# Kernel tuning notes

Measured on AMD Instinct MI355X. Metric: run time of the kernel, lower is better.

The kernel has to match this reference:

```python
import jax, jax.numpy as jnp
import numpy as np

B, S, N, H, E = 512, 96, 64, 512, 512  # batch, seq_len, nodes(c_in), hidden, edges/graph


def setup_inputs() -> dict:
    key = jax.random.key(0)
    ks = jax.random.split(key, 6)
    x = jax.random.normal(ks[0], (B, S, N), jnp.float32)
    edge_index = jax.random.randint(ks[1], (B, 2, E), 0, N, dtype=jnp.int32)
    W1 = jax.random.normal(ks[2], (H, S), jnp.float32) * 0.05   # gcn1 lin weight [out,in]
    b1 = jnp.zeros((H,), jnp.float32)
    W2 = jax.random.normal(ks[3], (S, H), jnp.float32) * 0.05   # gcn2 lin weight
    b2 = jnp.zeros((S,), jnp.float32)
    conv_w = jax.random.normal(ks[4], (H, N, 3), jnp.float32) * 0.05  # Conv1d [out,in,k]
    return {"x": x, "edge_index": edge_index, "W1": W1, "b1": b1,
            "W2": W2, "b2": b2, "conv_w": conv_w}


def _gcn(h, src, dst, W, b, n):
    # PyG GCNConv: h' = D^-1/2 (A+I) D^-1/2 (h W^T) + b  (self-loops already in src/dst)
    h = h @ W.T                                       # [n, out]
    ones = jnp.ones(src.shape[0], h.dtype)
    deg = jax.ops.segment_sum(ones, dst, num_segments=n)
    dinv = jnp.where(deg > 0, jax.lax.rsqrt(deg), 0.0)
    norm = dinv[src] * dinv[dst]                      # [e]
    out = jax.ops.segment_sum(h[src] * norm[:, None], dst, num_segments=n)
    return out + b


def reference(x, edge_index, W1, b1, W2, b2, conv_w):
    b, s, n = x.shape
    loops = jnp.broadcast_to(jnp.arange(n, dtype=edge_index.dtype), (b, n))
    src = jnp.concatenate([edge_index[:, 0, :], loops], axis=1)  # add self-loops
    dst = jnp.concatenate([edge_index[:, 1, :], loops], axis=1)

    def per_graph(xb, sb, db):
        h = _gcn(xb.T, sb, db, W1, b1, n)   # [n, H]
        h = jax.nn.relu(h)
        h = _gcn(h, sb, db, W2, b2, n)      # [n, s]
        return h                             # channels-first [c_in, L]

    h = jax.vmap(per_graph)(x, src, dst)    # [b, n, s]
    # TokenEmbedding: Conv1d kernel=3, circular padding=1, no bias
    hp = jnp.pad(h, ((0, 0), (0, 0), (1, 1)), mode='wrap')
    y = jax.lax.conv_general_dilated(hp, conv_w, (1,), 'VALID',
                                     dimension_numbers=('NCH', 'OIH', 'NCH'))  # [b, H, s]
    return jnp.transpose(y, (0, 2, 1))      # [b, s, H]; dropout = identity (eval)
```

## Files before the change

### kernel.cpp

```cpp
#include <hip/hip_runtime.h>
#include <hip/hip_bf16.h>

#define BB 512
#define SS 96
#define NN 64
#define HH 512
#define EE 512

typedef __attribute__((ext_vector_type(8))) short short8;
typedef __attribute__((ext_vector_type(4))) float f32x4;
typedef unsigned short u16;

__device__ __forceinline__ u16 f2bf(float f) {
    union { float f; unsigned u; } v; v.f = f;
    return (u16)((v.u + 0x7FFFu + ((v.u >> 16) & 1u)) >> 16);
}
__device__ __forceinline__ short8 ld8bf(const u16* p) { return *(const short8*)p; }
__device__ __forceinline__ short8 cvt8(const float* p) {
    float4 a = *(const float4*)p, b = *(const float4*)(p + 4);
    short8 r;
    r[0] = (short)f2bf(a.x); r[1] = (short)f2bf(a.y);
    r[2] = (short)f2bf(a.z); r[3] = (short)f2bf(a.w);
    r[4] = (short)f2bf(b.x); r[5] = (short)f2bf(b.y);
    r[6] = (short)f2bf(b.z); r[7] = (short)f2bf(b.w);
    return r;
}
__device__ __forceinline__ ushort4 packbf(f32x4 a) {
    ushort4 u; u.x = f2bf(a[0]); u.y = f2bf(a[1]); u.z = f2bf(a[2]); u.w = f2bf(a[3]);
    return u;
}

__global__ __launch_bounds__(256) void k_prep(const float* __restrict__ W1,
                                              const float* __restrict__ W2,
                                              const float* __restrict__ cw,
                                              u16* __restrict__ W1b,
                                              u16* __restrict__ W2b,
                                              u16* __restrict__ Wcb) {
    const int i0 = blockIdx.x * 256 + threadIdx.x, stp = gridDim.x * 256;
    for (int i = i0; i < HH * SS; i += stp) W1b[i] = f2bf(W1[i]);
    for (int i = i0; i < SS * HH; i += stp) W2b[i] = f2bf(W2[i]);
    for (int i = i0; i < HH * 192; i += stp) {
        int h = i / 192, q = i % 192, n = q / 3, kw = q % 3;
        Wcb[h * 192 + kw * 64 + n] = f2bf(cw[i]);
    }
}

__global__ __launch_bounds__(256) void k_all(const float* __restrict__ x,
                                             const int* __restrict__ ei,
                                             const u16* __restrict__ W1b,
                                             const float* __restrict__ b1,
                                             const u16* __restrict__ W2b,
                                             const float* __restrict__ b2,
                                             const u16* __restrict__ Wcb,
                                             float* __restrict__ out) {
    const int b = blockIdx.x, t = threadIdx.x;
    const int w = t >> 6, lane = t & 63, quad = lane >> 4, l16 = lane & 15;

    __shared__ __align__(16) char smem[59680];
    u16*   As   = (u16*)smem;
    u16*   Gs   = (u16*)(smem + 9216);
    u16*   H1c  = (u16*)(smem + 22528);
    u16*   Ts   = (u16*)(smem + 31744);
    u16*   Hp   = (u16*)(smem + 45568);
    float* Asm  = (float*)(smem + 31744);
    int*   deg  = (int*)smem;
    float* dinv = (float*)(smem + 256);

    for (int i = t; i < 4096; i += 256) Asm[i] = 0.f;
    if (t < 64) deg[t] = 1;
    __syncthreads();
    const int* eb = ei + (size_t)b * 2 * EE;
    for (int e = t; e < EE; e += 256) atomicAdd(&deg[eb[EE + e]], 1);
    __syncthreads();
    if (t < 64) dinv[t] = rsqrtf((float)deg[t]);
    __syncthreads();
    for (int e = t; e < EE; e += 256) {
        int s = eb[e], d = eb[EE + e];
        atomicAdd(&Asm[d * 64 + s], dinv[s] * dinv[d]);
    }
    if (t < 64) atomicAdd(&Asm[t * 64 + t], dinv[t] * dinv[t]);
    __syncthreads();
    for (int i = t; i < 1024; i += 256) {
        int n = i >> 4, m4 = (i & 15) * 4;
        f32x4 v = *(const f32x4*)(Asm + n * 64 + m4);
        *(ushort4*)(As + n * 72 + m4) = packbf(v);
    }
    __syncthreads();

    {
        short8 bf0[2];
        #pragma unroll
        for (int kc = 0; kc < 2; ++kc)
            bf0[kc] = ld8bf(As + (w * 16 + l16) * 72 + kc * 32 + quad * 8);
        const float* xb = x + (size_t)b * SS * NN;
        #pragma unroll
        for (int j = 0; j < 6; ++j) {
            f32x4 acc = (f32x4){0.f, 0.f, 0.f, 0.f};
            #pragma unroll
            for (int kc = 0; kc < 2; ++kc) {
                short8 a = cvt8(xb + (j * 16 + l16) * 64 + kc * 32 + quad * 8);
                acc = __builtin_amdgcn_mfma_f32_16x16x32_bf16(a, bf0[kc], acc, 0, 0, 0);
            }
            *(ushort4*)(Gs + (w * 16 + l16) * 104 + j * 16 + quad * 4) = packbf(acc);
        }
    }

    f32x4 accT[6];
    #pragma unroll
    for (int j = 0; j < 6; ++j) accT[j] = (f32x4){0.f, 0.f, 0.f, 0.f};

    for (int hc = 0; hc < 8; ++hc) {
        short8 gb[3];
        #pragma unroll
        for (int kc = 0; kc < 3; ++kc)
            gb[kc] = ld8bf(Gs + (w * 16 + l16) * 104 + kc * 32 + quad * 8);
        #pragma unroll
        for (int hs = 0; hs < 4; ++hs) {
            f32x4 a1 = (f32x4){0.f, 0.f, 0.f, 0.f};
            #pragma unroll
            for (int kc = 0; kc < 3; ++kc) {
                short8 wa = ld8bf(W1b + (size_t)(hc * 64 + hs * 16 + l16) * 96 + kc * 32 + quad * 8);
                a1 = __builtin_amdgcn_mfma_f32_16x16x32_bf16(wa, gb[kc], a1, 0, 0, 0);
            }
            float4 bias = *(const float4*)(b1 + hc * 64 + hs * 16 + quad * 4);
            f32x4 r;
            r[0] = fmaxf(a1[0] + bias.x, 0.f); r[1] = fmaxf(a1[1] + bias.y, 0.f);
            r[2] = fmaxf(a1[2] + bias.z, 0.f); r[3] = fmaxf(a1[3] + bias.w, 0.f);
            *(ushort4*)(H1c + (w * 16 + l16) * 72 + hs * 16 + quad * 4) = packbf(r);
        }
        short8 ha[2];
        #pragma unroll
        for (int kc = 0; kc < 2; ++kc)
            ha[kc] = ld8bf(H1c + (w * 16 + l16) * 72 + kc * 32 + quad * 8);
        #pragma unroll
        for (int j = 0; j < 6; ++j)
            #pragma unroll
            for (int kc = 0; kc < 2; ++kc) {
                short8 wb = ld8bf(W2b + (size_t)(j * 16 + l16) * HH + hc * 64 + kc * 32 + quad * 8);
                accT[j] = __builtin_amdgcn_mfma_f32_16x16x32_bf16(ha[kc], wb, accT[j], 0, 0, 0);
            }
    }

    #pragma unroll
    for (int j = 0; j < 6; ++j)
        *(ushort4*)(Ts + (j * 16 + l16) * 72 + w * 16 + quad * 4) = packbf(accT[j]);
    __syncthreads();

    {
        short8 af[2];
        #pragma unroll
        for (int kc = 0; kc < 2; ++kc)
            af[kc] = ld8bf(As + (w * 16 + l16) * 72 + kc * 32 + quad * 8);
        #pragma unroll
        for (int j = 0; j < 6; ++j) {
            f32x4 a3 = (f32x4){0.f, 0.f, 0.f, 0.f};
            #pragma unroll
            for (int kc = 0; kc < 2; ++kc) {
                short8 tb = ld8bf(Ts + (j * 16 + l16) * 72 + kc * 32 + quad * 8);
                a3 = __builtin_amdgcn_mfma_f32_16x16x32_bf16(af[kc], tb, a3, 0, 0, 0);
            }
            float bs = b2[j * 16 + l16];
            f32x4 r = {a3[0] + bs, a3[1] + bs, a3[2] + bs, a3[3] + bs};
            *(ushort4*)(Hp + (j * 16 + l16 + 1) * 72 + w * 16 + quad * 4) = packbf(r);
        }
    }
    __syncthreads();
    if (t < 64) {
        Hp[t] = Hp[96 * 72 + t];
        Hp[97 * 72 + t] = Hp[72 + t];
    }
    __syncthreads();

    float* ob = out + (size_t)b * SS * HH;
    for (int ht = 0; ht < 8; ++ht) {
        short8 wa[6];
        #pragma unroll
        for (int kc = 0; kc < 6; ++kc)
            wa[kc] = ld8bf(Wcb + (size_t)(ht * 64 + w * 16 + l16) * 192 + kc * 32 + quad * 8);
        #pragma unroll
        for (int j = 0; j < 6; ++j) {
            f32x4 acc = (f32x4){0.f, 0.f, 0.f, 0.f};
            #pragma unroll
            for (int kc = 0; kc < 6; ++kc) {
                int kw = kc >> 1, nb = (kc & 1) * 32;
                short8 hb = ld8bf(Hp + (j * 16 + l16 + kw) * 72 + nb + quad * 8);
                acc = __builtin_amdgcn_mfma_f32_16x16x32_bf16(wa[kc], hb, acc, 0, 0, 0);
            }
            float4 vv = {acc[0], acc[1], acc[2], acc[3]};
            *(float4*)(ob + (size_t)(j * 16 + l16) * HH + ht * 64 + w * 16 + quad * 4) = vv;
        }
    }
}

extern "C" void kernel_launch(void* const* d_in, const int* in_sizes, int n_in,
                              void* d_out, int out_size, void* d_ws, size_t ws_size,
                              hipStream_t stream) {
    const float* x  = (const float*)d_in[0];
    const int*   ei = (const int*)d_in[1];
    const float* W1 = (const float*)d_in[2];
    const float* b1 = (const float*)d_in[3];
    const float* W2 = (const float*)d_in[4];
    const float* b2 = (const float*)d_in[5];
    const float* cw = (const float*)d_in[6];
    float* out = (float*)d_out;

    char* wsp = (char*)d_ws;
    u16* W1b = (u16*)wsp;
    u16* W2b = (u16*)(wsp + 98304);
    u16* Wcb = (u16*)(wsp + 196608);

    k_prep<<<96, 256, 0, stream>>>(W1, W2, cw, W1b, W2b, Wcb);
    k_all <<<BB, 256, 0, stream>>>(x, ei, W1b, b1, W2b, b2, Wcb, out);
}
```

Before: 172.8 us.

## Split fused kernel into GCN and conv kernels with wider conv grid

The single per-graph kernel is split in two. The GCN kernel writes the second-layer output in bf16 to a global workspace. A separate conv kernel then runs on a 4x512 grid, with each block handling 128 output channels, and rebuilds the circular padding when it loads into shared memory. The aim is more parallelism and occupancy in the output-bound conv stage, and a smaller LDS footprint for the GCN kernel. The cost is an extra launch plus a global round trip of the intermediate, about 6 MB written and read.

```diff
diff --git a/kernel.cpp b/kernel.cpp
--- a/kernel.cpp
+++ b/kernel.cpp
@@ -45,24 +45,22 @@
     }
 }
 
-__global__ __launch_bounds__(256) void k_all(const float* __restrict__ x,
+__global__ __launch_bounds__(256) void k_gcn(const float* __restrict__ x,
                                              const int* __restrict__ ei,
                                              const u16* __restrict__ W1b,
                                              const float* __restrict__ b1,
                                              const u16* __restrict__ W2b,
                                              const float* __restrict__ b2,
-                                             const u16* __restrict__ Wcb,
-                                             float* __restrict__ out) {
+                                             u16* __restrict__ H2T) {
     const int b = blockIdx.x, t = threadIdx.x;
     const int w = t >> 6, lane = t & 63, quad = lane >> 4, l16 = lane & 15;
 
-    __shared__ __align__(16) char smem[59680];
+    __shared__ __align__(16) char smem[46080];
     u16*   As   = (u16*)smem;
     u16*   Gs   = (u16*)(smem + 9216);
     u16*   H1c  = (u16*)(smem + 22528);
     u16*   Ts   = (u16*)(smem + 31744);
-    u16*   Hp   = (u16*)(smem + 45568);
-    float* Asm  = (float*)(smem + 31744);
+    float* Asm  = (float*)(smem + 29696);
     int*   deg  = (int*)smem;
     float* dinv = (float*)(smem + 256);
 
@@ -151,6 +149,7 @@
         #pragma unroll
         for (int kc = 0; kc < 2; ++kc)
             af[kc] = ld8bf(As + (w * 16 + l16) * 72 + kc * 32 + quad * 8);
+        u16* Hb = H2T + (size_t)b * SS * NN;
         #pragma unroll
         for (int j = 0; j < 6; ++j) {
             f32x4 a3 = (f32x4){0.f, 0.f, 0.f, 0.f};
@@ -161,33 +160,46 @@
             }
             float bs = b2[j * 16 + l16];
             f32x4 r = {a3[0] + bs, a3[1] + bs, a3[2] + bs, a3[3] + bs};
-            *(ushort4*)(Hp + (j * 16 + l16 + 1) * 72 + w * 16 + quad * 4) = packbf(r);
-        }
-    }
-    __syncthreads();
-    if (t < 64) {
-        Hp[t] = Hp[96 * 72 + t];
-        Hp[97 * 72 + t] = Hp[72 + t];
+            *(ushort4*)(Hb + (j * 16 + l16) * NN + w * 16 + quad * 4) = packbf(r);
+        }
+    }
+}
+
+__global__ __launch_bounds__(256, 6) void k_conv(const u16* __restrict__ H2T,
+                                                 const u16* __restrict__ Wcb,
+                                                 float* __restrict__ out) {
+    const int hb = blockIdx.x, b = blockIdx.y, t = threadIdx.x;
+    const int w = t >> 6, lane = t & 63, quad = lane >> 4, l16 = lane & 15;
+
+    __shared__ __align__(16) u16 Hp[98 * 72];
+
+    const u16* Hsrc = H2T + (size_t)b * SS * NN;
+    for (int i = t; i < 98 * 8; i += 256) {
+        int sp = i >> 3, c8 = (i & 7) * 8;
+        int s = (sp == 0) ? 95 : ((sp == 97) ? 0 : sp - 1);
+        *(short8*)(Hp + sp * 72 + c8) = *(const short8*)(Hsrc + s * NN + c8);
     }
     __syncthreads();
 
     float* ob = out + (size_t)b * SS * HH;
-    for (int ht = 0; ht < 8; ++ht) {
+    #pragma unroll
+    for (int ht = 0; ht < 2; ++ht) {
+        const int h0 = hb * 128 + w * 32 + ht * 16;
         short8 wa[6];
         #pragma unroll
         for (int kc = 0; kc < 6; ++kc)
-            wa[kc] = ld8bf(Wcb + (size_t)(ht * 64 + w * 16 + l16) * 192 + kc * 32 + quad * 8);
+            wa[kc] = ld8bf(Wcb + (size_t)(h0 + l16) * 192 + kc * 32 + quad * 8);
         #pragma unroll
         for (int j = 0; j < 6; ++j) {
             f32x4 acc = (f32x4){0.f, 0.f, 0.f, 0.f};
             #pragma unroll
             for (int kc = 0; kc < 6; ++kc) {
                 int kw = kc >> 1, nb = (kc & 1) * 32;
-                short8 hb = ld8bf(Hp + (j * 16 + l16 + kw) * 72 + nb + quad * 8);
-                acc = __builtin_amdgcn_mfma_f32_16x16x32_bf16(wa[kc], hb, acc, 0, 0, 0);
+                short8 hb8 = ld8bf(Hp + (j * 16 + l16 + kw) * 72 + nb + quad * 8);
+                acc = __builtin_amdgcn_mfma_f32_16x16x32_bf16(wa[kc], hb8, acc, 0, 0, 0);
             }
             float4 vv = {acc[0], acc[1], acc[2], acc[3]};
-            *(float4*)(ob + (size_t)(j * 16 + l16) * HH + ht * 64 + w * 16 + quad * 4) = vv;
+            *(float4*)(ob + (size_t)(j * 16 + l16) * HH + h0 + quad * 4) = vv;
         }
     }
 }
@@ -205,10 +217,13 @@
     float* out = (float*)d_out;
 
     char* wsp = (char*)d_ws;
-    u16* W1b = (u16*)wsp;
-    u16* W2b = (u16*)(wsp + 98304);
-    u16* Wcb = (u16*)(wsp + 196608);
+    u16* H2T = (u16*)wsp;
+    u16* W1b = (u16*)(wsp + 6291456);
+    u16* W2b = (u16*)(wsp + 6389760);
+    u16* Wcb = (u16*)(wsp + 6488064);
 
     k_prep<<<96, 256, 0, stream>>>(W1, W2, cw, W1b, W2b, Wcb);
-    k_all <<<BB, 256, 0, stream>>>(x, ei, W1b, b1, W2b, b2, Wcb, out);
-}
+    k_gcn <<<BB, 256, 0, stream>>>(x, ei, W1b, b1, W2b, b2, H2T);
+    dim3 gc(4, BB);
+    k_conv<<<gc, 256, 0, stream>>>(H2T, Wcb, out);
+}
```

After: 181.8 us. 5.2% more time.
